# Kernel tuning notes

Hardware: AMD Instinct MI355X
Metric: run time of the kernel (lower is better)

Reference implementation:

```python
import jax, jax.numpy as jnp
import numpy as np

B, N, K = 4, 4096, 16
C_IN, C_OUT = 128, 128
H1, H2 = 256, 256
IN_SZ = 2 * C_IN  # key_feats='self' -> concat(self feats, neighbor feats)


def setup_inputs() -> dict:
    key = jax.random.key(0)
    ks = jax.random.split(key, 12)
    s = 1.0 / np.sqrt(IN_SZ)
    inp = {
        "keys": jax.random.normal(ks[0], (B, N, 3), jnp.float32),
        "points": jax.random.normal(ks[1], (B, N, 3), jnp.float32),
        "feats": jax.random.normal(ks[2], (B, N, C_IN), jnp.float32),
        "n_idxs": jax.random.randint(ks[3], (B, N, K), 0, N, jnp.int32),
        "neighbor_valid": jax.random.randint(ks[4], (B, N, K), 0, 2, jnp.int32),
        "W1": jax.random.uniform(ks[5], (IN_SZ, H1), jnp.float32, -s, s),
        "b1": jnp.zeros((H1,), jnp.float32),
        "W2": jax.random.uniform(ks[6], (H1, H2), jnp.float32, -1/np.sqrt(H1), 1/np.sqrt(H1)),
        "b2": jnp.zeros((H2,), jnp.float32),
        "W3": jax.random.uniform(ks[7], (H2, C_OUT), jnp.float32, -1/np.sqrt(H2), 1/np.sqrt(H2)),
        "b3": jnp.zeros((C_OUT,), jnp.float32),
    }
    return inp


def reference(keys, points, feats, n_idxs, neighbor_valid, W1, b1, W2, b2, W3, b3):
    # gather neighbor features: feats[bb, n_idxs] -> [B, N, K, C_IN]
    bb = jnp.arange(feats.shape[0])[:, None, None]
    neighbor_feats = feats[bb, n_idxs]
    # key_feats='self': broadcast query's own feats over neighbor dim, concat
    exp_feats = jnp.broadcast_to(feats[:, :, None, :], neighbor_feats.shape)
    pairs = jnp.concatenate([exp_feats, neighbor_feats], axis=-1)  # [B,N,K,2C]
    # SetTransform MLP per edge (reduction='none')
    h = jax.nn.relu(jnp.einsum("bnki,ih->bnkh", pairs, W1) + b1)
    h = jax.nn.relu(jnp.einsum("bnkh,hj->bnkj", h, W2) + b2)
    edges = jnp.einsum("bnkj,jo->bnko", h, W3) + b3  # [B,N,K,C_OUT]
    # mask invalid neighbors and reduce over neighbor dim
    mask = neighbor_valid[..., None].astype(edges.dtype)
    reduced = jnp.sum(edges * mask, axis=2)  # [B,N,C_OUT]
    return reduced
```

## Files before the change

kernel.cpp:

```cpp
#include <hip/hip_runtime.h>
#include <stdint.h>

#define Cc 128

typedef __attribute__((ext_vector_type(4))) float f32x4;
typedef __attribute__((ext_vector_type(8))) short s16x8;

__device__ __forceinline__ unsigned int asu(float f) { union { float f; unsigned int u; } v; v.f = f; return v.u; }
__device__ __forceinline__ float asf(unsigned int u) { union { unsigned int u; float f; } v; v.u = u; return v.f; }

__device__ __forceinline__ unsigned short f2bf_rne(float f) {
  unsigned int u = asu(f);
  unsigned int r = u + 0x7FFFu + ((u >> 16) & 1u);
  return (unsigned short)(r >> 16);
}

__device__ __forceinline__ unsigned int pk2(float lo, float hi) {
  return __builtin_amdgcn_perm(asu(hi) + 0x8000u, asu(lo) + 0x8000u, 0x07060302u);
}

__device__ __forceinline__ unsigned int cvt1(unsigned int a, unsigned int b) {
  float alo = asf(a << 16), ahi = asf(a & 0xFFFF0000u);
  float blo = asf(b << 16), bhi = asf(b & 0xFFFF0000u);
  float lo = fmaxf(alo + blo, 0.f);
  float hi = fmaxf(ahi + bhi, 0.f);
  return pk2(lo, hi);
}

#define MFMA16(a, b, c) __builtin_amdgcn_mfma_f32_16x16x32_bf16((a), (b), (c), 0, 0, 0)

__global__ void pack_kernel(const float* __restrict__ W1,
                            const float* __restrict__ W2,
                            const float* __restrict__ W3,
                            const float* __restrict__ b2,
                            const float* __restrict__ b3,
                            unsigned short* __restrict__ W1p,
                            unsigned short* __restrict__ W2p,
                            unsigned short* __restrict__ W3p,
                            float* __restrict__ t3v,
                            float* __restrict__ u3v) {
  int blk = blockIdx.x, t = threadIdx.x;
  if (blk < 32) {
    int f = blk * 256 + t;
    int l = f & 63, ct = (f >> 6) & 31, kt = f >> 11;
    int col = ct * 16 + (l & 15);
    int k0 = kt * 32 + ((l >> 4) << 3);
    unsigned short tmp[8];
#pragma unroll
    for (int j = 0; j < 8; ++j) {
      int k = k0 + j;
      float v = (col < 256) ? W1[k * 256 + col] : W1[(128 + k) * 256 + (col - 256)];
      tmp[j] = f2bf_rne(v);
    }
    *(uint4*)(W1p + f * 8) = *(uint4*)tmp;
  } else if (blk < 64) {
    int f = (blk - 32) * 256 + t;
    int l = f & 63, ct = (f >> 6) & 15, kt = f >> 10;
    int col = ct * 16 + (l & 15);
    int k0 = kt * 32 + ((l >> 4) << 3);
    unsigned short tmp[8];
#pragma unroll
    for (int j = 0; j < 8; ++j) tmp[j] = f2bf_rne(W2[(k0 + j) * 256 + col]);
    *(uint4*)(W2p + f * 8) = *(uint4*)tmp;
  } else if (blk < 80) {
    int f = (blk - 64) * 256 + t;
    int l = f & 63, ct = (f >> 6) & 7, kt = f >> 9;
    int col = ct * 16 + (l & 15);
    int k0 = kt * 32 + ((l >> 4) << 3);
    unsigned short tmp[8];
#pragma unroll
    for (int j = 0; j < 8; ++j) tmp[j] = f2bf_rne(W3[(k0 + j) * 128 + col]);
    *(uint4*)(W3p + f * 8) = *(uint4*)tmp;
  } else {
    if (t < 128) {
      float s = 0.f;
      for (int j = 0; j < 256; ++j) s += fmaxf(b2[j], 0.f) * W3[j * 128 + t];
      t3v[t] = b3[t] + s;
      u3v[t] = 16.f * s;
    }
  }
}

__global__ __launch_bounds__(256, 2) void k1_gemm(
    const float* __restrict__ feats,
    const unsigned short* __restrict__ W1p,
    const float* __restrict__ b1,
    unsigned short* __restrict__ A_ws,
    unsigned short* __restrict__ B_ws) {
  __shared__ __attribute__((aligned(16))) unsigned short cs[64 * 512];
  char* cb = (char*)cs;
  int m0 = blockIdx.x * 64;
  int t = threadIdx.x, w = t >> 6, l = t & 63, lr = l & 15, lg = l >> 4;
  f32x4 zero4 = {0.f, 0.f, 0.f, 0.f};
  f32x4 acc[4][8];
#pragma unroll
  for (int i = 0; i < 4; ++i)
#pragma unroll
    for (int j = 0; j < 8; ++j) acc[i][j] = zero4;

  for (int kt = 0; kt < 4; ++kt) {
    s16x8 a[4];
#pragma unroll
    for (int rt = 0; rt < 4; ++rt) {
      const float* fr = feats + (m0 + rt * 16 + lr) * 128 + kt * 32 + lg * 8;
      float4 f0 = *(const float4*)fr;
      float4 f1 = *(const float4*)(fr + 4);
      uint4 pk;
      pk.x = pk2(f0.x, f0.y);
      pk.y = pk2(f0.z, f0.w);
      pk.z = pk2(f1.x, f1.y);
      pk.w = pk2(f1.z, f1.w);
      *(uint4*)&a[rt] = pk;
    }
#pragma unroll
    for (int ctl = 0; ctl < 8; ++ctl) {
      s16x8 bf = *(const s16x8*)(W1p + (((kt * 32) + (w * 8 + ctl)) * 64 + l) * 8);
#pragma unroll
      for (int rt = 0; rt < 4; ++rt)
        acc[rt][ctl] = MFMA16(a[rt], bf, acc[rt][ctl]);
    }
  }

#pragma unroll
  for (int ctl = 0; ctl < 8; ++ctl) {
    int col = w * 128 + ctl * 16 + lr;
    float bias = (col < 256) ? b1[col] : 0.f;
#pragma unroll
    for (int rt = 0; rt < 4; ++rt) {
#pragma unroll
      for (int reg = 0; reg < 4; ++reg) {
        int node = rt * 16 + lg * 4 + reg;
        float v = acc[rt][ctl][reg] + bias;
        unsigned short bv = (unsigned short)((asu(v) + 0x8000u) >> 16);
        *(unsigned short*)(cb + ((node * 1024 + col * 2) ^ ((node & 7) << 4))) = bv;
      }
    }
  }
  __syncthreads();
#pragma unroll
  for (int i = 0; i < 16; ++i) {
    int row = i * 4 + w;
    uint4 v = *(const uint4*)(cb + row * 1024 + ((l * 16) ^ ((row & 7) << 4)));
    int node = m0 + row;
    unsigned short* dst = (l < 32) ? (A_ws + node * 256 + l * 8)
                                   : (B_ws + node * 256 + (l - 32) * 8);
    *(uint4*)dst = v;
  }
}

__global__ __launch_bounds__(512, 4) void k2_fused(
    const unsigned short* __restrict__ A_ws,
    const unsigned short* __restrict__ B_ws,
    const unsigned short* __restrict__ W2p,
    const unsigned short* __restrict__ W3p,
    const int* __restrict__ n_idxs,
    const int* __restrict__ valid,
    const float* __restrict__ b2,
    const float* __restrict__ t3v,
    const float* __restrict__ u3v,
    float* __restrict__ out) {
  __shared__ __attribute__((aligned(16))) unsigned short h1s[128 * 128];
  __shared__ __attribute__((aligned(16))) unsigned short gs[16 * 264];
  __shared__ float nvf[8];
  char* h1b = (char*)h1s;
  char* gb = (char*)gs;

  int t = threadIdx.x;
  int w = t >> 6, l = t & 63, lr = l & 15, lg = l >> 4;
  int wg = blockIdx.x;
  int qbase = wg * 8, ebase = wg * 128;
  int bN = qbase & ~4095;

  if (t < 256) {
    int row = 8 + (t >> 5), ch = t & 31;
    *(f32x4*)(gb + row * 528 + ch * 16) = f32x4{0.f, 0.f, 0.f, 0.f};
  }
  if (t < 8) {
    int s = 0;
#pragma unroll
    for (int k = 0; k < 16; ++k) s += valid[ebase + t * 16 + k];
    nvf[t] = (float)s;
  }

  int r = t >> 2, sub = t & 3;
  int nb = n_idxs[ebase + r];
  bool vld = valid[ebase + r] != 0;
  const unsigned short* pa = A_ws + (qbase + (r >> 4)) * 256 + sub * 32;
  const unsigned short* pb = B_ws + (bN + nb) * 256 + sub * 32;
  int wbase = r * 256 + sub * 64;
  int swz = (r & 7) << 4;
  int rswz = (lr & 7) << 4;

  f32x4 zero4 = {0.f, 0.f, 0.f, 0.f};
  f32x4 acc[8][2];
#pragma unroll
  for (int i = 0; i < 8; ++i) {
    acc[i][0] = zero4;
    acc[i][1] = zero4;
  }

  for (int p = 0; p < 2; ++p) {
#pragma unroll
    for (int i = 0; i < 4; ++i) {
      uint4 av = *(const uint4*)(pa + p * 128 + i * 8);
      uint4 bv = *(const uint4*)(pb + p * 128 + i * 8);
      uint4 o;
      o.x = cvt1(av.x, bv.x);
      o.y = cvt1(av.y, bv.y);
      o.z = cvt1(av.z, bv.z);
      o.w = cvt1(av.w, bv.w);
      if (!vld) { o.x = 0u; o.y = 0u; o.z = 0u; o.w = 0u; }
      *(uint4*)(h1b + ((wbase + i * 16) ^ swz)) = o;
    }
    __syncthreads();
#pragma unroll
    for (int kt = 0; kt < 4; ++kt) {
      s16x8 a[8];
      int kofs = (kt * 64 + lg * 16) ^ rswz;
#pragma unroll
      for (int rt = 0; rt < 8; ++rt)
        a[rt] = *(const s16x8*)(h1b + (rt * 16 + lr) * 256 + kofs);
      int ktg = p * 4 + kt;
#pragma unroll
      for (int ctl = 0; ctl < 2; ++ctl) {
        s16x8 bf = *(const s16x8*)(W2p + (((ktg * 16) + (w * 2 + ctl)) * 64 + l) * 8);
#pragma unroll
        for (int rt = 0; rt < 8; ++rt)
          acc[rt][ctl] = MFMA16(a[rt], bf, acc[rt][ctl]);
      }
    }
    __syncthreads();
  }

  float bias0 = b2[w * 32 + lr];
  float bias1 = b2[w * 32 + 16 + lr];
#pragma unroll
  for (int ctl = 0; ctl < 2; ++ctl) {
    int col = w * 32 + ctl * 16 + lr;
    float bias = ctl ? bias1 : bias0;
#pragma unroll
    for (int rt = 0; rt < 8; ++rt) {
      float s = fmaxf(acc[rt][ctl][0] + bias, 0.f)
              + fmaxf(acc[rt][ctl][1] + bias, 0.f)
              + fmaxf(acc[rt][ctl][2] + bias, 0.f)
              + fmaxf(acc[rt][ctl][3] + bias, 0.f);
      s += __shfl_xor(s, 16);
      s += __shfl_xor(s, 32);
      if (l < 16)
        *(unsigned short*)(gb + rt * 528 + col * 2) = f2bf_rne(s);
    }
  }
  __syncthreads();

  f32x4 acc3 = zero4;
#pragma unroll
  for (int kt = 0; kt < 8; ++kt) {
    s16x8 a = *(const s16x8*)(gb + lr * 528 + kt * 64 + lg * 16);
    s16x8 bf = *(const s16x8*)(W3p + ((kt * 8 + w) * 64 + l) * 8);
    acc3 = MFMA16(a, bf, acc3);
  }
  int col = w * 16 + lr;
  if (lg < 2) {
    float tt = t3v[col], uu = u3v[col];
#pragma unroll
    for (int reg = 0; reg < 4; ++reg) {
      int q = lg * 4 + reg;
      out[(qbase + q) * Cc + col] = acc3[reg] + nvf[q] * tt - uu;
    }
  }
}

extern "C" void kernel_launch(void* const* d_in, const int* in_sizes, int n_in,
                              void* d_out, int out_size, void* d_ws, size_t ws_size,
                              hipStream_t stream) {
  const float* feats = (const float*)d_in[2];
  const int* n_idxs = (const int*)d_in[3];
  const int* valid = (const int*)d_in[4];
  const float* W1 = (const float*)d_in[5];
  const float* b1 = (const float*)d_in[6];
  const float* W2 = (const float*)d_in[7];
  const float* b2 = (const float*)d_in[8];
  const float* W3 = (const float*)d_in[9];
  const float* b3 = (const float*)d_in[10];
  float* out = (float*)d_out;

  char* ws = (char*)d_ws;
  unsigned short* A_ws = (unsigned short*)(ws);
  unsigned short* B_ws = (unsigned short*)(ws + (8u << 20));
  unsigned short* W1p  = (unsigned short*)(ws + (16u << 20));
  unsigned short* W2p  = (unsigned short*)(ws + (16u << 20) + (128u << 10));
  unsigned short* W3p  = (unsigned short*)(ws + (16u << 20) + (256u << 10));
  float* t3v = (float*)(ws + (16u << 20) + (320u << 10));
  float* u3v = (float*)(ws + (16u << 20) + (321u << 10));

  pack_kernel<<<81, 256, 0, stream>>>(W1, W2, W3, b2, b3, W1p, W2p, W3p, t3v, u3v);
  k1_gemm<<<256, 256, 0, stream>>>(feats, W1p, b1, A_ws, B_ws);
  k2_fused<<<2048, 512, 0, stream>>>(A_ws, B_ws, W2p, W3p, n_idxs, valid, b2, t3v, u3v, out);
}
```

Baseline: 160.0 us.

## Switch edge MLP layer-2 to 32x32 MFMA with 4 queries per block

The fused edge kernel now processes 4 queries (64 edges) per workgroup instead of 8. It builds the full 256-wide h1 tile in shared memory in one pass and computes layer 2 with 32x32x16 bf16 MFMAs, with each wave owning 32 output columns. W2 is repacked to match the 32x32 operand layout. This removes the two-pass loop and its extra barriers and reuses each B fragment across two A tiles. The cost is twice as many workgroups, so fixed per-block work (bias loads, W3 stage, output writes) is repeated more often and the final 16x16 MFMA stage wastes more of its padded rows. The bias-constant precompute in the pack kernel is also split across 256 threads.

Measured after the change: 175.0 us. 9.4% more time.

```diff
diff --git a/kernel.cpp b/kernel.cpp
--- a/kernel.cpp
+++ b/kernel.cpp
@@ -4,6 +4,7 @@
 #define Cc 128
 
 typedef __attribute__((ext_vector_type(4))) float f32x4;
+typedef __attribute__((ext_vector_type(16))) float f32x16;
 typedef __attribute__((ext_vector_type(8))) short s16x8;
 
 __device__ __forceinline__ unsigned int asu(float f) { union { float f; unsigned int u; } v; v.f = f; return v.u; }
@@ -28,6 +29,7 @@
 }
 
 #define MFMA16(a, b, c) __builtin_amdgcn_mfma_f32_16x16x32_bf16((a), (b), (c), 0, 0, 0)
+#define MFMA32(a, b, c) __builtin_amdgcn_mfma_f32_32x32x16_bf16((a), (b), (c), 0, 0, 0)
 
 __global__ void pack_kernel(const float* __restrict__ W1,
                             const float* __restrict__ W2,
@@ -55,9 +57,9 @@
     *(uint4*)(W1p + f * 8) = *(uint4*)tmp;
   } else if (blk < 64) {
     int f = (blk - 32) * 256 + t;
-    int l = f & 63, ct = (f >> 6) & 15, kt = f >> 10;
-    int col = ct * 16 + (l & 15);
-    int k0 = kt * 32 + ((l >> 4) << 3);
+    int l = f & 63, ct = (f >> 6) & 7, kt = f >> 9;
+    int col = ct * 32 + (l & 31);
+    int k0 = kt * 16 + ((l >> 5) << 3);
     unsigned short tmp[8];
 #pragma unroll
     for (int j = 0; j < 8; ++j) tmp[j] = f2bf_rne(W2[(k0 + j) * 256 + col]);
@@ -72,11 +74,19 @@
     for (int j = 0; j < 8; ++j) tmp[j] = f2bf_rne(W3[(k0 + j) * 128 + col]);
     *(uint4*)(W3p + f * 8) = *(uint4*)tmp;
   } else {
+    __shared__ float part[256];
+    if (t < 256) {
+      int col = t & 127, half = t >> 7;
+      float s = 0.f;
+      for (int j = half * 128; j < half * 128 + 128; ++j)
+        s += fmaxf(b2[j], 0.f) * W3[j * 128 + col];
+      part[t] = s;
+    }
+    __syncthreads();
     if (t < 128) {
-      float s = 0.f;
-      for (int j = 0; j < 256; ++j) s += fmaxf(b2[j], 0.f) * W3[j * 128 + t];
-      t3v[t] = b3[t] + s;
-      u3v[t] = 16.f * s;
+      float c3 = part[t] + part[t + 128];
+      t3v[t] = b3[t] + c3;
+      u3v[t] = 16.f * c3;
     }
   }
 }
@@ -159,113 +169,109 @@
     const float* __restrict__ t3v,
     const float* __restrict__ u3v,
     float* __restrict__ out) {
-  __shared__ __attribute__((aligned(16))) unsigned short h1s[128 * 128];
+  __shared__ __attribute__((aligned(16))) unsigned short h1s[64 * 256];
   __shared__ __attribute__((aligned(16))) unsigned short gs[16 * 264];
-  __shared__ float nvf[8];
+  __shared__ float nvf[4];
   char* h1b = (char*)h1s;
   char* gb = (char*)gs;
 
-  int t = threadIdx.x;
-  int w = t >> 6, l = t & 63, lr = l & 15, lg = l >> 4;
+  int t = threadIdx.x, w = t >> 6, l = t & 63;
   int wg = blockIdx.x;
-  int qbase = wg * 8, ebase = wg * 128;
+  int qbase = wg * 4, ebase = wg * 64;
   int bN = qbase & ~4095;
 
-  if (t < 256) {
-    int row = 8 + (t >> 5), ch = t & 31;
+  if (t < 384) {
+    int row = 4 + (t >> 5), ch = t & 31;
     *(f32x4*)(gb + row * 528 + ch * 16) = f32x4{0.f, 0.f, 0.f, 0.f};
   }
-  if (t < 8) {
+  if (t < 4) {
     int s = 0;
 #pragma unroll
     for (int k = 0; k < 16; ++k) s += valid[ebase + t * 16 + k];
     nvf[t] = (float)s;
   }
 
-  int r = t >> 2, sub = t & 3;
-  int nb = n_idxs[ebase + r];
-  bool vld = valid[ebase + r] != 0;
-  const unsigned short* pa = A_ws + (qbase + (r >> 4)) * 256 + sub * 32;
-  const unsigned short* pb = B_ws + (bN + nb) * 256 + sub * 32;
-  int wbase = r * 256 + sub * 64;
-  int swz = (r & 7) << 4;
-  int rswz = (lr & 7) << 4;
-
-  f32x4 zero4 = {0.f, 0.f, 0.f, 0.f};
-  f32x4 acc[8][2];
-#pragma unroll
-  for (int i = 0; i < 8; ++i) {
-    acc[i][0] = zero4;
-    acc[i][1] = zero4;
-  }
-
-  for (int p = 0; p < 2; ++p) {
+  {
+    int r = t >> 3, c8 = t & 7;
+    int nb = n_idxs[ebase + r];
+    int vld = valid[ebase + r];
+    const unsigned short* pa = A_ws + (qbase + (r >> 4)) * 256;
+    const unsigned short* pb = B_ws + (bN + nb) * 256;
+    int swz = (r & 7) << 4;
 #pragma unroll
     for (int i = 0; i < 4; ++i) {
-      uint4 av = *(const uint4*)(pa + p * 128 + i * 8);
-      uint4 bv = *(const uint4*)(pb + p * 128 + i * 8);
+      int ch = c8 + i * 8;
+      uint4 av = *(const uint4*)(pa + ch * 8);
+      uint4 bv = *(const uint4*)(pb + ch * 8);
       uint4 o;
       o.x = cvt1(av.x, bv.x);
       o.y = cvt1(av.y, bv.y);
       o.z = cvt1(av.z, bv.z);
       o.w = cvt1(av.w, bv.w);
       if (!vld) { o.x = 0u; o.y = 0u; o.z = 0u; o.w = 0u; }
-      *(uint4*)(h1b + ((wbase + i * 16) ^ swz)) = o;
-    }
-    __syncthreads();
-#pragma unroll
-    for (int kt = 0; kt < 4; ++kt) {
-      s16x8 a[8];
-      int kofs = (kt * 64 + lg * 16) ^ rswz;
-#pragma unroll
-      for (int rt = 0; rt < 8; ++rt)
-        a[rt] = *(const s16x8*)(h1b + (rt * 16 + lr) * 256 + kofs);
-      int ktg = p * 4 + kt;
-#pragma unroll
-      for (int ctl = 0; ctl < 2; ++ctl) {
-        s16x8 bf = *(const s16x8*)(W2p + (((ktg * 16) + (w * 2 + ctl)) * 64 + l) * 8);
-#pragma unroll
-        for (int rt = 0; rt < 8; ++rt)
-          acc[rt][ctl] = MFMA16(a[rt], bf, acc[rt][ctl]);
-      }
-    }
-    __syncthreads();
-  }
-
-  float bias0 = b2[w * 32 + lr];
-  float bias1 = b2[w * 32 + 16 + lr];
-#pragma unroll
-  for (int ctl = 0; ctl < 2; ++ctl) {
-    int col = w * 32 + ctl * 16 + lr;
-    float bias = ctl ? bias1 : bias0;
-#pragma unroll
-    for (int rt = 0; rt < 8; ++rt) {
-      float s = fmaxf(acc[rt][ctl][0] + bias, 0.f)
-              + fmaxf(acc[rt][ctl][1] + bias, 0.f)
-              + fmaxf(acc[rt][ctl][2] + bias, 0.f)
-              + fmaxf(acc[rt][ctl][3] + bias, 0.f);
-      s += __shfl_xor(s, 16);
-      s += __shfl_xor(s, 32);
-      if (l < 16)
-        *(unsigned short*)(gb + rt * 528 + col * 2) = f2bf_rne(s);
+      *(uint4*)(h1b + ((r * 512 + ch * 16) ^ swz)) = o;
     }
   }
   __syncthreads();
 
-  f32x4 acc3 = zero4;
-#pragma unroll
-  for (int kt = 0; kt < 8; ++kt) {
-    s16x8 a = *(const s16x8*)(gb + lr * 528 + kt * 64 + lg * 16);
-    s16x8 bf = *(const s16x8*)(W3p + ((kt * 8 + w) * 64 + l) * 8);
-    acc3 = MFMA16(a, bf, acc3);
-  }
-  int col = w * 16 + lr;
-  if (lg < 2) {
-    float tt = t3v[col], uu = u3v[col];
-#pragma unroll
-    for (int reg = 0; reg < 4; ++reg) {
-      int q = lg * 4 + reg;
-      out[(qbase + q) * Cc + col] = acc3[reg] + nvf[q] * tt - uu;
+  f32x16 acc0 = {0.f,0.f,0.f,0.f,0.f,0.f,0.f,0.f,0.f,0.f,0.f,0.f,0.f,0.f,0.f,0.f};
+  f32x16 acc1 = acc0;
+  {
+    int hi = l >> 5, col = l & 31;
+    int row0 = col, row1 = 32 + col;
+    int base0 = row0 * 512, sz0 = (row0 & 7) << 4;
+    int base1 = row1 * 512, sz1 = (row1 & 7) << 4;
+#pragma unroll
+    for (int kt = 0; kt < 16; ++kt) {
+      int kb = kt * 32 + hi * 16;
+      s16x8 a0 = *(const s16x8*)(h1b + ((base0 + kb) ^ sz0));
+      s16x8 a1 = *(const s16x8*)(h1b + ((base1 + kb) ^ sz1));
+      s16x8 bf = *(const s16x8*)(W2p + ((kt * 8 + w) * 64 + l) * 8);
+      acc0 = MFMA32(a0, bf, acc0);
+      acc1 = MFMA32(a1, bf, acc1);
+    }
+  }
+
+  {
+    int col = l & 31;
+    float bias = b2[w * 32 + col];
+    float s0 = 0.f, s1 = 0.f, s2 = 0.f, s3 = 0.f;
+#pragma unroll
+    for (int g = 0; g < 8; ++g) {
+      s0 += fmaxf(acc0[g] + bias, 0.f);
+      s1 += fmaxf(acc0[8 + g] + bias, 0.f);
+      s2 += fmaxf(acc1[g] + bias, 0.f);
+      s3 += fmaxf(acc1[8 + g] + bias, 0.f);
+    }
+    s0 += __shfl_xor(s0, 32);
+    s1 += __shfl_xor(s1, 32);
+    s2 += __shfl_xor(s2, 32);
+    s3 += __shfl_xor(s3, 32);
+    if (l < 32) {
+      int cb2 = (w * 32 + col) * 2;
+      *(unsigned short*)(gb + 0 * 528 + cb2) = f2bf_rne(s0);
+      *(unsigned short*)(gb + 1 * 528 + cb2) = f2bf_rne(s1);
+      *(unsigned short*)(gb + 2 * 528 + cb2) = f2bf_rne(s2);
+      *(unsigned short*)(gb + 3 * 528 + cb2) = f2bf_rne(s3);
+    }
+  }
+  __syncthreads();
+
+  {
+    int lr = l & 15, lg = l >> 4;
+    f32x4 acc3 = {0.f, 0.f, 0.f, 0.f};
+#pragma unroll
+    for (int kt = 0; kt < 8; ++kt) {
+      s16x8 a = *(const s16x8*)(gb + lr * 528 + kt * 64 + lg * 16);
+      s16x8 bf = *(const s16x8*)(W3p + ((kt * 8 + w) * 64 + l) * 8);
+      acc3 = MFMA16(a, bf, acc3);
+    }
+    if (lg == 0) {
+      int col3 = w * 16 + lr;
+      float tt = t3v[col3], uu = u3v[col3];
+#pragma unroll
+      for (int reg = 0; reg < 4; ++reg)
+        out[(qbase + reg) * Cc + col3] = acc3[reg] + nvf[reg] * tt - uu;
     }
   }
 }
@@ -295,5 +301,5 @@
 
   pack_kernel<<<81, 256, 0, stream>>>(W1, W2, W3, b2, b3, W1p, W2p, W3p, t3v, u3v);
   k1_gemm<<<256, 256, 0, stream>>>(feats, W1p, b1, A_ws, B_ws);
-  k2_fused<<<2048, 512, 0, stream>>>(A_ws, B_ws, W2p, W3p, n_idxs, valid, b2, t3v, u3v, out);
-}
+  k2_fused<<<4096, 512, 0, stream>>>(A_ws, B_ws, W2p, W3p, n_idxs, valid, b2, t3v, u3v, out);
+}
```
